# Optimization experiments

Hardware: AMD Instinct MI355X
Metric: run time of the kernel (lower is better)

Reference implementation:

```python
import jax, jax.numpy as jnp
import numpy as np
from jax import lax

VOCAB, EMB, FILT, ATT, KW = 50000, 300, 400, 200, 3
B, N = 4096, 30

def setup_inputs() -> dict:
    key = jax.random.key(0)
    ks = jax.random.split(key, 7)
    encoded_title = jax.random.randint(ks[0], (B, N), 0, VOCAB)
    emb = jax.random.normal(ks[1], (VOCAB, EMB), dtype=jnp.float32) * 0.1
    conv_w = jax.random.normal(ks[2], (FILT, EMB, KW), dtype=jnp.float32) * (1.0 / np.sqrt(EMB * KW))
    conv_b = jnp.zeros((FILT,), dtype=jnp.float32)
    v = jax.random.normal(ks[3], (FILT, ATT), dtype=jnp.float32) * (1.0 / np.sqrt(FILT))
    vb = jnp.zeros((ATT,), dtype=jnp.float32)
    q = jax.random.normal(ks[4], (ATT, 1), dtype=jnp.float32) * (1.0 / np.sqrt(ATT))
    return {"encoded_title": encoded_title, "emb": emb, "conv_w": conv_w,
            "conv_b": conv_b, "v": v, "vb": vb, "q": q}

def reference(encoded_title, emb, conv_w, conv_b, v, vb, q):
    mask = (encoded_title != 0).astype(jnp.float32)          # [B, N]
    W = emb[encoded_title]                                    # [B, N, E]
    x = jnp.transpose(W, (0, 2, 1))                           # [B, E, N]
    C = lax.conv_general_dilated(x, conv_w, window_strides=(1,),
                                 padding=[(1, 1)],
                                 dimension_numbers=("NCH", "OIH", "NCH"))
    C = jnp.transpose(C, (0, 2, 1)) + conv_b                  # [B, N, F]
    C = jax.nn.relu(C)
    a = jnp.tanh(C @ v + vb)                                  # [B, N, A]
    a = (a @ q)[..., 0]                                       # [B, N]
    alpha = jax.nn.softmax(a, axis=0)                         # softmax over batch dim (faithful to dim=0)
    alpha = alpha * mask
    e = jnp.einsum("bn,bnf->bf", alpha, C)                    # batched weighted-sum pooling
    return e
```

## Files before the change

### kernel.cpp

```cpp
#include <hip/hip_runtime.h>
#include <hip/hip_bf16.h>

#define VOCAB 50000
#define EMB   300
#define FILT  400
#define ATT   200
#define BB    4096
#define NN    30

#define ATTP  208
#define KC    416

typedef short bf16x8 __attribute__((ext_vector_type(8)));
typedef float f32x4  __attribute__((ext_vector_type(4)));
typedef unsigned short u16x4 __attribute__((ext_vector_type(4)));

static __device__ __forceinline__ unsigned short f2bf(float f) {
    __hip_bfloat16 h = __float2bfloat16(f);
    union { __hip_bfloat16 h; unsigned short u; } c; c.h = h; return c.u;
}
static __device__ __forceinline__ float bf2f(unsigned short u) {
    union { unsigned int u; float f; } c; c.u = ((unsigned int)u) << 16; return c.f;
}
static __device__ __forceinline__ float fast_tanh(float x) {
    float e = __expf(2.f * x);
    return 1.f - 2.f * __builtin_amdgcn_rcpf(e + 1.f);
}

static __device__ __forceinline__ void dma16(const unsigned short* g, unsigned short* l) {
    __builtin_amdgcn_global_load_lds(
        (const __attribute__((address_space(1))) unsigned int*)(const void*)g,
        (__attribute__((address_space(3))) unsigned int*)(void*)l,
        16, 0, 0);
}

#define CFENCE() asm volatile("" ::: "memory")
static __device__ __forceinline__ void bar_lgkm0() {
    asm volatile("s_waitcnt lgkmcnt(0)" ::: "memory");
    __builtin_amdgcn_s_barrier();
    CFENCE();
}

__global__ __launch_bounds__(256) void kP(const float* __restrict__ conv_w,
                                          const float* __restrict__ v,
                                          const float* __restrict__ vb,
                                          const float* __restrict__ q,
                                          unsigned short* __restrict__ Bc2,
                                          unsigned short* __restrict__ Bv2,
                                          float* __restrict__ vbp,
                                          float* __restrict__ qp) {
    int t = blockIdx.x * 256 + threadIdx.x;
    const int NBC = 750 * 512;
    if (t < NBC) {
        int tau = t >> 9, off = t & 511;
        int l = off >> 3, j = off & 7;
        int lm = l & 15, qq = l >> 4;
        int ft = tau % 25, es = (tau / 25) % 10, k = tau / 250;
        int f = ft * 16 + lm;
        int e = es * 32 + qq * 8 + j;
        float val = (e < EMB) ? conv_w[((size_t)f * EMB + e) * 3 + k] : 0.f;
        Bc2[t] = f2bf(val);
    } else {
        int t2 = t - NBC;
        if (t2 < 169 * 512) {
            int tau = t2 >> 9, off = t2 & 511;
            int l = off >> 3, j = off & 7;
            int lm = l & 15, qq = l >> 4;
            int ks = tau / 13, at = tau % 13;
            int att = at * 16 + lm;
            int fcol = ks * 32 + qq * 8 + j;
            float val = (att < ATT && fcol < FILT) ? v[(size_t)fcol * ATT + att] : 0.f;
            Bv2[t2] = f2bf(val);
        }
    }
    if (t < ATTP) {
        vbp[t] = (t < ATT) ? vb[t] : 0.f;
        qp[t]  = (t < ATT) ? q[t] : 0.f;
    }
}

static __device__ __forceinline__ void gather16(const float* __restrict__ emb,
                                                int tok, int e0, float4* aR4) {
#pragma unroll
    for (int c = 0; c < 4; c++) {
        float4 z; z.x = 0.f; z.y = 0.f; z.z = 0.f; z.w = 0.f;
        int ee = e0 + c * 4;
        if (tok >= 0 && ee < EMB)
            z = *(const float4*)(emb + (size_t)tok * EMB + ee);
        aR4[c] = z;
    }
}

static __device__ __forceinline__ void publishA(unsigned short* Ab, int uj, int uh,
                                                const float4* aR4) {
    const float* af = (const float*)aR4;
    union { bf16x8 v; unsigned short u[8]; } cv0, cv1;
#pragma unroll
    for (int jj = 0; jj < 8; jj++) { cv0.u[jj] = f2bf(af[jj]); cv1.u[jj] = f2bf(af[8 + jj]); }
    *(bf16x8*)(Ab + uj * 40 + uh * 16) = cv0.v;
    *(bf16x8*)(Ab + uj * 40 + uh * 16 + 8) = cv1.v;
}

__global__ __launch_bounds__(640, 3) void k1_conv(
    const int* __restrict__ idx,
    const float* __restrict__ emb,
    const unsigned short* __restrict__ Bc2,
    const float* __restrict__ conv_b,
    unsigned short* __restrict__ Cws)
{
    extern __shared__ unsigned short sh[];
    unsigned short* const Bs = sh;
    unsigned short* const As = sh + 38400;

    const int bid = blockIdx.x;
    const int t = threadIdx.x;
    const int lane = t & 63, wave = t >> 6;
    const int lm = lane & 15, qq = lane >> 4;
    const int wg = wave / 5, fw = wave % 5;
    const int rbase = wg * 64;
    const bool stager = (wave < 5);

    const int g = t - 320;
    const int uj = g >> 1, uh = g & 1;
    const bool gact = (!stager) && (g < 262);
    int utok = -1;
    if (gact && uj < 128) {
        int ub = uj >> 5, uj2 = uj & 31;
        if (uj2 >= 1 && uj2 <= 30) utok = idx[(bid * 4 + ub) * NN + (uj2 - 1)];
    }

    float4 aR4[4];
    if (stager) {
#pragma unroll
        for (int s = 0; s < 3; s++) {
#pragma unroll
            for (int nt = 0; nt < 5; nt++) {
                int gt = (s * 10) * 25 + fw * 5 + nt;
                dma16(Bc2 + (size_t)gt * 512 + lane * 8,
                      Bs + s * 12800 + (fw * 5 + nt) * 512);
            }
        }
        asm volatile("s_waitcnt vmcnt(10)" ::: "memory");
    } else if (gact) {
        gather16(emb, utok, 0 + uh * 16, aR4);
        publishA(As, uj, uh, aR4);
        gather16(emb, utok, 32 + uh * 16, aR4);
        publishA(As + 5240, uj, uh, aR4);
        gather16(emb, utok, 64 + uh * 16, aR4);
    }

    f32x4 acc[4][5];
#pragma unroll
    for (int mt = 0; mt < 4; mt++)
#pragma unroll
        for (int nt = 0; nt < 5; nt++)
            acc[mt][nt] = (f32x4){0.f, 0.f, 0.f, 0.f};

    bar_lgkm0();

    for (int es = 0; es < 10; ++es) {
        const unsigned short* Ab = As + (es & 1) * 5240;
#pragma unroll
        for (int k = 0; k < 3; ++k) {
            const unsigned short* bb = Bs + k * 12800;
            bf16x8 aF[4];
#pragma unroll
            for (int mt = 0; mt < 4; mt++)
                aF[mt] = *(const bf16x8*)(Ab + (rbase + mt * 16 + lm + k) * 40 + qq * 8);
#pragma unroll
            for (int nt = 0; nt < 5; nt++) {
                bf16x8 bF = *(const bf16x8*)(bb + (fw * 5 + nt) * 512 + lane * 8);
#pragma unroll
                for (int mt = 0; mt < 4; mt++)
                    acc[mt][nt] = __builtin_amdgcn_mfma_f32_16x16x32_bf16(aF[mt], bF, acc[mt][nt], 0, 0, 0);
            }
            if (k == 0 && gact && es >= 1 && es <= 8) {
                publishA(As + ((es + 1) & 1) * 5240, uj, uh, aR4);
                if (es <= 7) gather16(emb, utok, (es + 2) * 32 + uh * 16, aR4);
            }
            if (stager) {
                if (es < 9 || k == 0)
                    asm volatile("s_waitcnt vmcnt(5)" ::: "memory");
                else if (k == 1)
                    asm volatile("s_waitcnt vmcnt(0)" ::: "memory");
            }
            if (es < 9 || k < 2) bar_lgkm0();
            if (stager && es < 9) {
#pragma unroll
                for (int nt = 0; nt < 5; nt++) {
                    int gt = (k * 10 + es + 1) * 25 + fw * 5 + nt;
                    dma16(Bc2 + (size_t)gt * 512 + lane * 8,
                          Bs + k * 12800 + (fw * 5 + nt) * 512);
                }
            }
        }
    }

    const int f0 = fw * 80;
    float cb[5];
#pragma unroll
    for (int nt = 0; nt < 5; nt++) cb[nt] = conv_b[f0 + nt * 16 + lm];
#pragma unroll
    for (int mt = 0; mt < 4; mt++) {
#pragma unroll
        for (int r = 0; r < 4; r++) {
            int lrow = rbase + mt * 16 + qq * 4 + r;
            int n = lrow & 31;
            int bglob = bid * 4 + (lrow >> 5);
            if (n < NN) {
#pragma unroll
                for (int nt = 0; nt < 5; nt++) {
                    float vv = fmaxf(acc[mt][nt][r] + cb[nt], 0.f);
                    Cws[((size_t)bglob * NN + n) * FILT + f0 + nt * 16 + lm] = f2bf(vv);
                }
            }
        }
    }
}

__global__ __launch_bounds__(256, 3) void k2_att(
    const unsigned short* __restrict__ Cws,
    const unsigned short* __restrict__ Bv2,
    const float* __restrict__ vbp, const float* __restrict__ qp,
    float* __restrict__ a_out)
{
    __shared__ unsigned short Bs[2 * 13 * 512];
    const int lane = threadIdx.x & 63;
    const int wave = threadIdx.x >> 6;
    const int lm = lane & 15, qq = lane >> 4;
    const int r0 = blockIdx.x * 128 + wave * 32;

#pragma unroll
    for (int s = 0; s < 2; s++)
#pragma unroll
        for (int nt = 0; nt < 13; nt++)
            if ((nt & 3) == wave)
                dma16(Bv2 + (size_t)(s * 13 + nt) * 512 + lane * 8,
                      Bs + s * 6656 + nt * 512);

    bf16x8 aFc[2], aFn[2];
#pragma unroll
    for (int mt = 0; mt < 2; mt++)
        aFc[mt] = *(const bf16x8*)(Cws + (size_t)(r0 + mt * 16 + lm) * FILT + 8 * qq);

    f32x4 acc[2][13];
#pragma unroll
    for (int mt = 0; mt < 2; mt++)
#pragma unroll
        for (int nt = 0; nt < 13; nt++) acc[mt][nt] = (f32x4){0.f, 0.f, 0.f, 0.f};

    __syncthreads();

    for (int ks = 0; ks < 13; ++ks) {
        if (ks < 12)
#pragma unroll
            for (int mt = 0; mt < 2; mt++)
                aFn[mt] = *(const bf16x8*)(Cws + (size_t)(r0 + mt * 16 + lm) * FILT + (ks + 1) * 32 + 8 * qq);
        const unsigned short* bb = Bs + (ks & 1) * 6656;
#pragma unroll
        for (int nt = 0; nt < 13; nt++) {
            bf16x8 bF = *(const bf16x8*)(bb + nt * 512 + lane * 8);
#pragma unroll
            for (int mt = 0; mt < 2; mt++)
                acc[mt][nt] = __builtin_amdgcn_mfma_f32_16x16x32_bf16(aFc[mt], bF, acc[mt][nt], 0, 0, 0);
        }
        __syncthreads();
        if (ks + 2 < 13)
#pragma unroll
            for (int nt = 0; nt < 13; nt++)
                if ((nt & 3) == wave)
                    dma16(Bv2 + (size_t)((ks + 2) * 13 + nt) * 512 + lane * 8,
                          Bs + (ks & 1) * 6656 + nt * 512);
#pragma unroll
        for (int mt = 0; mt < 2; mt++) aFc[mt] = aFn[mt];
    }

#pragma unroll
    for (int mt = 0; mt < 2; mt++) {
        float rs[4] = {0.f, 0.f, 0.f, 0.f};
#pragma unroll
        for (int nt = 0; nt < 13; nt++) {
            int att = nt * 16 + lm;
            float vbv = vbp[att], qv = qp[att];
#pragma unroll
            for (int r = 0; r < 4; r++)
                rs[r] += fast_tanh(acc[mt][nt][r] + vbv) * qv;
        }
#pragma unroll
        for (int off = 1; off < 16; off <<= 1)
#pragma unroll
            for (int r = 0; r < 4; r++) rs[r] += __shfl_xor(rs[r], off, 64);
        if (lm == 0) {
#pragma unroll
            for (int r = 0; r < 4; r++) {
                int rg = r0 + mt * 16 + qq * 4 + r;
                a_out[(size_t)(rg % NN) * BB + (rg / NN)] = rs[r];
            }
        }
    }
}

__global__ __launch_bounds__(1024) void k3_stats(const float* __restrict__ a,
                                                 float* __restrict__ mS) {
    int n = blockIdx.x, tid = threadIdx.x;
    float4 v4 = *(const float4*)(a + (size_t)n * BB + tid * 4);
    float m = fmaxf(fmaxf(v4.x, v4.y), fmaxf(v4.z, v4.w));
    __shared__ float red[32];
#pragma unroll
    for (int off = 32; off >= 1; off >>= 1) m = fmaxf(m, __shfl_xor(m, off, 64));
    int wv = tid >> 6;
    if ((tid & 63) == 0) red[wv] = m;
    __syncthreads();
#pragma unroll
    for (int w = 0; w < 16; w++) m = fmaxf(m, red[w]);
    float e0 = expf(v4.x - m), e1 = expf(v4.y - m);
    float e2 = expf(v4.z - m), e3 = expf(v4.w - m);
    float s = e0 + e1 + e2 + e3;
#pragma unroll
    for (int off = 32; off >= 1; off >>= 1) s += __shfl_xor(s, off, 64);
    if ((tid & 63) == 0) red[16 + wv] = s;
    __syncthreads();
    s = 0.f;
#pragma unroll
    for (int w = 0; w < 16; w++) s += red[16 + w];
    if (tid == 0) { mS[n] = m; mS[NN + n] = s; }
}

__global__ __launch_bounds__(128) void k4_pool(
    const float* __restrict__ a, const float* __restrict__ mS,
    const int* __restrict__ idx, const unsigned short* __restrict__ C,
    float* __restrict__ out)
{
    int b = blockIdx.x;
    int tid = threadIdx.x;
    __shared__ float al[NN];
    if (tid < NN) {
        float av = a[(size_t)tid * BB + b];
        float msk = (idx[(size_t)b * NN + tid] != 0) ? 1.f : 0.f;
        al[tid] = expf(av - mS[tid]) * (1.f / mS[NN + tid]) * msk;
    }
    __syncthreads();
    if (tid < 100) {
        int f = tid * 4;
        float s0 = 0.f, s1 = 0.f, s2 = 0.f, s3 = 0.f;
        const unsigned short* Cb = C + (size_t)b * (NN * FILT) + f;
#pragma unroll
        for (int n = 0; n < NN; n++) {
            u16x4 c = *(const u16x4*)(Cb + (size_t)n * FILT);
            float aa = al[n];
            s0 = fmaf(aa, bf2f(c[0]), s0);
            s1 = fmaf(aa, bf2f(c[1]), s1);
            s2 = fmaf(aa, bf2f(c[2]), s2);
            s3 = fmaf(aa, bf2f(c[3]), s3);
        }
        float4 o; o.x = s0; o.y = s1; o.z = s2; o.w = s3;
        *(float4*)(out + (size_t)b * FILT + f) = o;
    }
}

extern "C" void kernel_launch(void* const* d_in, const int* in_sizes, int n_in,
                              void* d_out, int out_size, void* d_ws, size_t ws_size,
                              hipStream_t stream) {
    const int*   idx    = (const int*)d_in[0];
    const float* emb    = (const float*)d_in[1];
    const float* conv_w = (const float*)d_in[2];
    const float* conv_b = (const float*)d_in[3];
    const float* v      = (const float*)d_in[4];
    const float* vb     = (const float*)d_in[5];
    const float* q      = (const float*)d_in[6];
    float* out = (float*)d_out;

    char* ws = (char*)d_ws;
    size_t o = 0;
    unsigned short* Bv2 = (unsigned short*)(ws + o); o += (size_t)169 * 512 * 2;
    float* vbp = (float*)(ws + o);                   o += 1024;
    float* qp  = (float*)(ws + o);                   o += 1024;
    float* mS  = (float*)(ws + o);                   o += 1024;
    unsigned short* Bc2 = (unsigned short*)(ws + o);
    float* a_buf = (float*)(ws + o);
    o += (size_t)750 * 512 * 2;
    unsigned short* Cws = (unsigned short*)(ws + o);

    static bool s_attr_set = false;
    if (!s_attr_set) {
        hipFuncSetAttribute(reinterpret_cast<const void*>(k1_conv),
                            hipFuncAttributeMaxDynamicSharedMemorySize, 98304);
        s_attr_set = true;
    }

    const int NP = 750 * 512 + 169 * 512;
    kP<<<(NP + 255) / 256, 256, 0, stream>>>(conv_w, v, vb, q, Bc2, Bv2, vbp, qp);
    k1_conv<<<BB / 4, 640, 97760, stream>>>(idx, emb, Bc2, conv_b, Cws);
    k2_att<<<(BB * NN) / 128, 256, 0, stream>>>(Cws, Bv2, vbp, qp, a_buf);
    k3_stats<<<NN, 1024, 0, stream>>>(a_buf, mS);
    k4_pool<<<BB, 128, 0, stream>>>(a_buf, mS, idx, Cws, out);
}
```

Before: 269.9 us.

## Warp-specialize conv kernel: preload full A tile, dedicated DMA waves double-buffer B

All threads now gather the whole embedding A tile (all 10 E-slabs) into LDS up front instead of streaming it across iterations. Two dedicated loader waves then double-buffer the conv-weight B slices while ten compute waves run MFMA at raised priority. The intent is to stop compute waves from doing DMA and gather work and to simplify the pipeline. In exchange, LDS use grows to about 156KB per block, which allows only one block per CU. The upfront gather is also fully exposed latency.

```diff
diff --git a/kernel.cpp b/kernel.cpp
--- a/kernel.cpp
+++ b/kernel.cpp
@@ -79,29 +79,7 @@
     }
 }
 
-static __device__ __forceinline__ void gather16(const float* __restrict__ emb,
-                                                int tok, int e0, float4* aR4) {
-#pragma unroll
-    for (int c = 0; c < 4; c++) {
-        float4 z; z.x = 0.f; z.y = 0.f; z.z = 0.f; z.w = 0.f;
-        int ee = e0 + c * 4;
-        if (tok >= 0 && ee < EMB)
-            z = *(const float4*)(emb + (size_t)tok * EMB + ee);
-        aR4[c] = z;
-    }
-}
-
-static __device__ __forceinline__ void publishA(unsigned short* Ab, int uj, int uh,
-                                                const float4* aR4) {
-    const float* af = (const float*)aR4;
-    union { bf16x8 v; unsigned short u[8]; } cv0, cv1;
-#pragma unroll
-    for (int jj = 0; jj < 8; jj++) { cv0.u[jj] = f2bf(af[jj]); cv1.u[jj] = f2bf(af[8 + jj]); }
-    *(bf16x8*)(Ab + uj * 40 + uh * 16) = cv0.v;
-    *(bf16x8*)(Ab + uj * 40 + uh * 16 + 8) = cv1.v;
-}
-
-__global__ __launch_bounds__(640, 3) void k1_conv(
+__global__ __launch_bounds__(768, 3) void k1_conv(
     const int* __restrict__ idx,
     const float* __restrict__ emb,
     const unsigned short* __restrict__ Bc2,
@@ -109,44 +87,60 @@
     unsigned short* __restrict__ Cws)
 {
     extern __shared__ unsigned short sh[];
-    unsigned short* const Bs = sh;
-    unsigned short* const As = sh + 38400;
+    unsigned short* const As = sh;
+    unsigned short* const Bs = sh + 52400;
 
     const int bid = blockIdx.x;
     const int t = threadIdx.x;
     const int lane = t & 63, wave = t >> 6;
     const int lm = lane & 15, qq = lane >> 4;
+    const bool comp = (wave < 10);
     const int wg = wave / 5, fw = wave % 5;
     const int rbase = wg * 64;
-    const bool stager = (wave < 5);
-
-    const int g = t - 320;
-    const int uj = g >> 1, uh = g & 1;
-    const bool gact = (!stager) && (g < 262);
-    int utok = -1;
-    if (gact && uj < 128) {
-        int ub = uj >> 5, uj2 = uj & 31;
-        if (uj2 >= 1 && uj2 <= 30) utok = idx[(bid * 4 + ub) * NN + (uj2 - 1)];
-    }
-
-    float4 aR4[4];
-    if (stager) {
-#pragma unroll
-        for (int s = 0; s < 3; s++) {
-#pragma unroll
-            for (int nt = 0; nt < 5; nt++) {
-                int gt = (s * 10) * 25 + fw * 5 + nt;
-                dma16(Bc2 + (size_t)gt * 512 + lane * 8,
-                      Bs + s * 12800 + (fw * 5 + nt) * 512);
-            }
-        }
-        asm volatile("s_waitcnt vmcnt(10)" ::: "memory");
-    } else if (gact) {
-        gather16(emb, utok, 0 + uh * 16, aR4);
-        publishA(As, uj, uh, aR4);
-        gather16(emb, utok, 32 + uh * 16, aR4);
-        publishA(As + 5240, uj, uh, aR4);
-        gather16(emb, utok, 64 + uh * 16, aR4);
+    const int ft0 = (wave == 10) ? 0 : 13;
+    const int ftn = (wave == 10) ? 13 : 12;
+
+    for (int u = t; u < 1310; u += 768) {
+        int row = u / 10, c = u % 10;
+        int tok = -1;
+        if (row < 128) {
+            int pos = row & 31;
+            if (pos >= 1 && pos <= 30) tok = idx[(bid * 4 + (row >> 5)) * NN + (pos - 1)];
+        }
+        float vals[32];
+#pragma unroll
+        for (int q4 = 0; q4 < 8; q4++) {
+            float4 z; z.x = 0.f; z.y = 0.f; z.z = 0.f; z.w = 0.f;
+            int ee = c * 32 + q4 * 4;
+            if (tok >= 0 && ee < EMB)
+                z = *(const float4*)(emb + (size_t)tok * EMB + ee);
+            vals[q4 * 4 + 0] = z.x; vals[q4 * 4 + 1] = z.y;
+            vals[q4 * 4 + 2] = z.z; vals[q4 * 4 + 3] = z.w;
+        }
+        unsigned short* dst = As + c * 5240 + row * 40;
+#pragma unroll
+        for (int h = 0; h < 4; h++) {
+            union { bf16x8 v; unsigned short us[8]; } cv;
+#pragma unroll
+            for (int j = 0; j < 8; j++) cv.us[j] = f2bf(vals[h * 8 + j]);
+            *(bf16x8*)(dst + h * 8) = cv.v;
+        }
+    }
+
+    if (!comp) {
+#pragma unroll
+        for (int s = 0; s < 2; s++) {
+#pragma unroll
+            for (int i = 0; i < 13; i++) {
+                if (i < ftn) {
+                    int ft = ft0 + i;
+                    int gt = (s * 10) * 25 + ft;
+                    dma16(Bc2 + (size_t)gt * 512 + lane * 8,
+                          Bs + s * 12800 + ft * 512);
+                }
+            }
+        }
+        asm volatile("s_waitcnt vmcnt(0)" ::: "memory");
     }
 
     f32x4 acc[4][5];
@@ -159,59 +153,62 @@
     bar_lgkm0();
 
     for (int es = 0; es < 10; ++es) {
-        const unsigned short* Ab = As + (es & 1) * 5240;
+        const unsigned short* Ab = As + es * 5240;
 #pragma unroll
         for (int k = 0; k < 3; ++k) {
-            const unsigned short* bb = Bs + k * 12800;
-            bf16x8 aF[4];
-#pragma unroll
-            for (int mt = 0; mt < 4; mt++)
-                aF[mt] = *(const bf16x8*)(Ab + (rbase + mt * 16 + lm + k) * 40 + qq * 8);
-#pragma unroll
-            for (int nt = 0; nt < 5; nt++) {
-                bf16x8 bF = *(const bf16x8*)(bb + (fw * 5 + nt) * 512 + lane * 8);
+            const int s = es * 3 + k;
+            if (comp) {
+                const unsigned short* bb = Bs + (s & 1) * 12800;
+                bf16x8 aF[4];
 #pragma unroll
                 for (int mt = 0; mt < 4; mt++)
-                    acc[mt][nt] = __builtin_amdgcn_mfma_f32_16x16x32_bf16(aF[mt], bF, acc[mt][nt], 0, 0, 0);
-            }
-            if (k == 0 && gact && es >= 1 && es <= 8) {
-                publishA(As + ((es + 1) & 1) * 5240, uj, uh, aR4);
-                if (es <= 7) gather16(emb, utok, (es + 2) * 32 + uh * 16, aR4);
-            }
-            if (stager) {
-                if (es < 9 || k == 0)
-                    asm volatile("s_waitcnt vmcnt(5)" ::: "memory");
-                else if (k == 1)
-                    asm volatile("s_waitcnt vmcnt(0)" ::: "memory");
-            }
-            if (es < 9 || k < 2) bar_lgkm0();
-            if (stager && es < 9) {
+                    aF[mt] = *(const bf16x8*)(Ab + (rbase + mt * 16 + lm + k) * 40 + qq * 8);
+                __builtin_amdgcn_s_setprio(1);
 #pragma unroll
                 for (int nt = 0; nt < 5; nt++) {
-                    int gt = (k * 10 + es + 1) * 25 + fw * 5 + nt;
-                    dma16(Bc2 + (size_t)gt * 512 + lane * 8,
-                          Bs + k * 12800 + (fw * 5 + nt) * 512);
+                    bf16x8 bF = *(const bf16x8*)(bb + (fw * 5 + nt) * 512 + lane * 8);
+#pragma unroll
+                    for (int mt = 0; mt < 4; mt++)
+                        acc[mt][nt] = __builtin_amdgcn_mfma_f32_16x16x32_bf16(aF[mt], bF, acc[mt][nt], 0, 0, 0);
                 }
-            }
-        }
-    }
-
-    const int f0 = fw * 80;
-    float cb[5];
-#pragma unroll
-    for (int nt = 0; nt < 5; nt++) cb[nt] = conv_b[f0 + nt * 16 + lm];
-#pragma unroll
-    for (int mt = 0; mt < 4; mt++) {
-#pragma unroll
-        for (int r = 0; r < 4; r++) {
-            int lrow = rbase + mt * 16 + qq * 4 + r;
-            int n = lrow & 31;
-            int bglob = bid * 4 + (lrow >> 5);
-            if (n < NN) {
-#pragma unroll
-                for (int nt = 0; nt < 5; nt++) {
-                    float vv = fmaxf(acc[mt][nt][r] + cb[nt], 0.f);
-                    Cws[((size_t)bglob * NN + n) * FILT + f0 + nt * 16 + lm] = f2bf(vv);
+                __builtin_amdgcn_s_setprio(0);
+            } else if (s < 29) {
+                asm volatile("s_waitcnt vmcnt(0)" ::: "memory");
+            }
+            if (s < 29) bar_lgkm0();
+            if (!comp && s + 2 < 30) {
+                const int s2 = s + 2, es2 = s2 / 3, k2 = s2 - es2 * 3;
+#pragma unroll
+                for (int i = 0; i < 13; i++) {
+                    if (i < ftn) {
+                        int ft = ft0 + i;
+                        int gt = (k2 * 10 + es2) * 25 + ft;
+                        dma16(Bc2 + (size_t)gt * 512 + lane * 8,
+                              Bs + (s & 1) * 12800 + ft * 512);
+                    }
+                }
+            }
+        }
+    }
+
+    if (comp) {
+        const int f0 = fw * 80;
+        float cb[5];
+#pragma unroll
+        for (int nt = 0; nt < 5; nt++) cb[nt] = conv_b[f0 + nt * 16 + lm];
+#pragma unroll
+        for (int mt = 0; mt < 4; mt++) {
+#pragma unroll
+            for (int r = 0; r < 4; r++) {
+                int lrow = rbase + mt * 16 + qq * 4 + r;
+                int n = lrow & 31;
+                int bglob = bid * 4 + (lrow >> 5);
+                if (n < NN) {
+#pragma unroll
+                    for (int nt = 0; nt < 5; nt++) {
+                        float vv = fmaxf(acc[mt][nt][r] + cb[nt], 0.f);
+                        Cws[((size_t)bglob * NN + n) * FILT + f0 + nt * 16 + lm] = f2bf(vv);
+                    }
                 }
             }
         }
@@ -384,13 +381,13 @@
     static bool s_attr_set = false;
     if (!s_attr_set) {
         hipFuncSetAttribute(reinterpret_cast<const void*>(k1_conv),
-                            hipFuncAttributeMaxDynamicSharedMemorySize, 98304);
+                            hipFuncAttributeMaxDynamicSharedMemorySize, 156000);
         s_attr_set = true;
     }
 
     const int NP = 750 * 512 + 169 * 512;
     kP<<<(NP + 255) / 256, 256, 0, stream>>>(conv_w, v, vb, q, Bc2, Bv2, vbp, qp);
-    k1_conv<<<BB / 4, 640, 97760, stream>>>(idx, emb, Bc2, conv_b, Cws);
+    k1_conv<<<BB / 4, 768, 156000, stream>>>(idx, emb, Bc2, conv_b, Cws);
     k2_att<<<(BB * NN) / 128, 256, 0, stream>>>(Cws, Bv2, vbp, qp, a_buf);
     k3_stats<<<NN, 1024, 0, stream>>>(a_buf, mS);
     k4_pool<<<BB, 128, 0, stream>>>(a_buf, mS, idx, Cws, out);
```

Result: slower. 306.2 us (+13.5%).

## Read conv weights directly from global memory instead of staging them in LDS

Applied to the files above, without the earlier changes.

Drops the DMA staging of conv-weight B-tiles into shared memory and has each wave load its bf16 B fragments straight from global (L2-cached) memory. The embedding gather is now done by the first 262 threads rather than a dedicated half of the block, and per-k barriers are cut to one barrier per K-step. LDS use falls to just the double-buffered A tile, which permits more resident blocks. The cost is global-load latency on the MFMA critical path, partly hidden with s_setprio around the MFMA bursts.

```diff
diff --git a/kernel.cpp b/kernel.cpp
--- a/kernel.cpp
+++ b/kernel.cpp
@@ -108,21 +108,16 @@
     const float* __restrict__ conv_b,
     unsigned short* __restrict__ Cws)
 {
-    extern __shared__ unsigned short sh[];
-    unsigned short* const Bs = sh;
-    unsigned short* const As = sh + 38400;
-
+    __shared__ unsigned short As[2][131 * 40];
     const int bid = blockIdx.x;
     const int t = threadIdx.x;
     const int lane = t & 63, wave = t >> 6;
     const int lm = lane & 15, qq = lane >> 4;
     const int wg = wave / 5, fw = wave % 5;
     const int rbase = wg * 64;
-    const bool stager = (wave < 5);
-
-    const int g = t - 320;
-    const int uj = g >> 1, uh = g & 1;
-    const bool gact = (!stager) && (g < 262);
+
+    const int uj = t >> 1, uh = t & 1;
+    const bool gact = (t < 262);
     int utok = -1;
     if (gact && uj < 128) {
         int ub = uj >> 5, uj2 = uj & 31;
@@ -130,23 +125,10 @@
     }
 
     float4 aR4[4];
-    if (stager) {
-#pragma unroll
-        for (int s = 0; s < 3; s++) {
-#pragma unroll
-            for (int nt = 0; nt < 5; nt++) {
-                int gt = (s * 10) * 25 + fw * 5 + nt;
-                dma16(Bc2 + (size_t)gt * 512 + lane * 8,
-                      Bs + s * 12800 + (fw * 5 + nt) * 512);
-            }
-        }
-        asm volatile("s_waitcnt vmcnt(10)" ::: "memory");
-    } else if (gact) {
-        gather16(emb, utok, 0 + uh * 16, aR4);
-        publishA(As, uj, uh, aR4);
+    if (gact) {
+        gather16(emb, utok, uh * 16, aR4);
+        publishA(&As[0][0], uj, uh, aR4);
         gather16(emb, utok, 32 + uh * 16, aR4);
-        publishA(As + 5240, uj, uh, aR4);
-        gather16(emb, utok, 64 + uh * 16, aR4);
     }
 
     f32x4 acc[4][5];
@@ -159,41 +141,28 @@
     bar_lgkm0();
 
     for (int es = 0; es < 10; ++es) {
-        const unsigned short* Ab = As + (es & 1) * 5240;
+        const unsigned short* Ab = &As[es & 1][0];
+        if (gact && es < 9) publishA(&As[(es + 1) & 1][0], uj, uh, aR4);
+
 #pragma unroll
         for (int k = 0; k < 3; ++k) {
-            const unsigned short* bb = Bs + k * 12800;
             bf16x8 aF[4];
 #pragma unroll
             for (int mt = 0; mt < 4; mt++)
                 aF[mt] = *(const bf16x8*)(Ab + (rbase + mt * 16 + lm + k) * 40 + qq * 8);
+            const unsigned short* bg = Bc2 + ((size_t)((k * 10 + es) * 25) << 9) + lane * 8;
+            __builtin_amdgcn_s_setprio(1);
 #pragma unroll
             for (int nt = 0; nt < 5; nt++) {
-                bf16x8 bF = *(const bf16x8*)(bb + (fw * 5 + nt) * 512 + lane * 8);
+                bf16x8 bF = *(const bf16x8*)(bg + ((fw * 5 + nt) << 9));
 #pragma unroll
                 for (int mt = 0; mt < 4; mt++)
                     acc[mt][nt] = __builtin_amdgcn_mfma_f32_16x16x32_bf16(aF[mt], bF, acc[mt][nt], 0, 0, 0);
             }
-            if (k == 0 && gact && es >= 1 && es <= 8) {
-                publishA(As + ((es + 1) & 1) * 5240, uj, uh, aR4);
-                if (es <= 7) gather16(emb, utok, (es + 2) * 32 + uh * 16, aR4);
-            }
-            if (stager) {
-                if (es < 9 || k == 0)
-                    asm volatile("s_waitcnt vmcnt(5)" ::: "memory");
-                else if (k == 1)
-                    asm volatile("s_waitcnt vmcnt(0)" ::: "memory");
-            }
-            if (es < 9 || k < 2) bar_lgkm0();
-            if (stager && es < 9) {
-#pragma unroll
-                for (int nt = 0; nt < 5; nt++) {
-                    int gt = (k * 10 + es + 1) * 25 + fw * 5 + nt;
-                    dma16(Bc2 + (size_t)gt * 512 + lane * 8,
-                          Bs + k * 12800 + (fw * 5 + nt) * 512);
-                }
-            }
-        }
+            __builtin_amdgcn_s_setprio(0);
+        }
+        if (gact && es < 8) gather16(emb, utok, (es + 2) * 32 + uh * 16, aR4);
+        if (es < 9) bar_lgkm0();
     }
 
     const int f0 = fw * 80;
@@ -381,16 +350,9 @@
     o += (size_t)750 * 512 * 2;
     unsigned short* Cws = (unsigned short*)(ws + o);
 
-    static bool s_attr_set = false;
-    if (!s_attr_set) {
-        hipFuncSetAttribute(reinterpret_cast<const void*>(k1_conv),
-                            hipFuncAttributeMaxDynamicSharedMemorySize, 98304);
-        s_attr_set = true;
-    }
-
     const int NP = 750 * 512 + 169 * 512;
     kP<<<(NP + 255) / 256, 256, 0, stream>>>(conv_w, v, vb, q, Bc2, Bv2, vbp, qp);
-    k1_conv<<<BB / 4, 640, 97760, stream>>>(idx, emb, Bc2, conv_b, Cws);
+    k1_conv<<<BB / 4, 640, 0, stream>>>(idx, emb, Bc2, conv_b, Cws);
     k2_att<<<(BB * NN) / 128, 256, 0, stream>>>(Cws, Bv2, vbp, qp, a_buf);
     k3_stats<<<NN, 1024, 0, stream>>>(a_buf, mS);
     k4_pool<<<BB, 128, 0, stream>>>(a_buf, mS, idx, Cws, out);
```

New measurement: 313.6 us. +16.2%, slower.
